# Kernel optimization log

Measured on AMD Instinct MI355X. Metric: run time of the kernel, lower is better.

The kernel has to match this reference:

```python
import jax, jax.numpy as jnp
import numpy as np

BSZ, L, P, H = 8, 8192, 128, 128


def setup_inputs() -> dict:
    key = jax.random.key(0)
    ks = jax.random.split(key, 7)
    x = jax.random.normal(ks[0], (BSZ, L, H), jnp.float32)
    A_diag = jax.random.uniform(ks[1], (P,), jnp.float32, 0.0, 2.0)
    G_diag = jax.random.uniform(ks[2], (P,), jnp.float32, 0.0, 1.0)
    dt = jax.random.normal(ks[3], (P,), jnp.float32)
    B = jax.random.uniform(ks[4], (P, H, 2), jnp.float32, -1.0, 1.0) / np.sqrt(H)
    C = jax.random.uniform(ks[5], (H, P, 2), jnp.float32, -1.0, 1.0) / np.sqrt(P)
    D = jax.random.normal(ks[6], (H,), jnp.float32)
    return {"x": x, "A_diag": A_diag, "G_diag": G_diag, "dt": dt, "B": B, "C": C, "D": D}


def _project_G(G, A, dt):
    # clamp G >= 0 and fold A into the valid stability interval [A_low, A_high]
    G = jnp.maximum(G, 0.0)
    dt2 = jnp.maximum(dt ** 2, 1e-06)
    s = jnp.sqrt(1.0 + dt * G)
    A_low = (2.0 + dt * G - 2.0 * s) / dt2
    A_high = (2.0 + dt * G + 2.0 * s) / dt2
    A_proj = A_low + jax.nn.relu(A - A_low) - jax.nn.relu(A - A_high)
    return A_proj, G


def _binop(q_i, q_j):
    # 2x2 block (per diagonal state p) recurrence composition: M_j @ M_i
    A_i, b_i = q_i
    A_j, b_j = q_j
    A_new = jnp.einsum('...ikp,...kjp->...ijp', A_j, A_i)
    b_new = jnp.einsum('...ikp,...kp->...ip', A_j, b_i) + b_j
    return A_new, b_new


def reference(x, A_diag, G_diag, dt, B, C, D):
    # _project_A_dt
    dt_s = jax.nn.sigmoid(dt)                       # (P,)
    A = jnp.maximum(A_diag, 0.0)
    # G_base = projected G given (A, dt)
    _, G_base = _project_G(G_diag, A, dt_s)
    # constant damping: G_seq is G_base broadcast over time, then re-projected per step
    G_seq = jnp.broadcast_to(G_base, (L, P))        # (L,P)
    A_seq, G_seq = _project_G(G_seq, A, dt_s)       # broadcasts over L
    A_fin = jnp.min(A_seq, axis=0)                  # (P,)
    # complex input projection Bu_k = B_complex @ u_k
    Bc = B[..., 0] + 1j * B[..., 1]                 # (P,H)
    Cc = C[..., 0] + 1j * C[..., 1]                 # (H,P)
    Bu = jnp.einsum('blh,ph->blp', x, Bc)           # (BSZ,L,P) complex64
    # IMEX transition coefficients
    S = 1.0 + dt_s * G_seq                          # (L,P)
    M11 = 1.0 / S
    M12 = -(dt_s / S) * A_fin
    M21 = dt_s / S
    M22 = 1.0 - (dt_s ** 2 / S) * A_fin
    M = jnp.stack([jnp.stack([M11, M12], axis=-2),
                   jnp.stack([M21, M22], axis=-2)], axis=-3)   # (L,2,2,P) real
    F = jnp.stack([(dt_s / S) * Bu, (dt_s ** 2 / S) * Bu], axis=-2)  # (BSZ,L,2,P) complex
    M_b = jnp.broadcast_to(M, (BSZ,) + M.shape)     # (BSZ,L,2,2,P)
    _, xs = jax.lax.associative_scan(_binop, (M_b, F), axis=1)
    ys = xs[..., 1, :]                              # (BSZ,L,P) complex: x-component
    out = jnp.einsum('blp,hp->blh', ys, Cc).real + D * x
    return out
```

## Files before the change

kernel.cpp:

```cpp
#include <hip/hip_runtime.h>
#include <math.h>

#define BSZ_ 8
#define LEN_ 8192
#define NC_  128
#define CT_  64

typedef __attribute__((ext_vector_type(8))) short bf16x8;
typedef __attribute__((ext_vector_type(4))) float f32x4;
typedef __attribute__((ext_vector_type(4))) unsigned short u16x4;
typedef __attribute__((ext_vector_type(8))) unsigned short u16x8;

#define OFF_PRM 0
#define OFF_W1T 2048
#define OFF_W2T (OFF_W1T + 16384)
#define OFF_MPW (OFF_W2T + 16384)
#define OFF_SUM (OFF_MPW + 16384)
#define OFF_V2  (OFF_SUM + BSZ_*NC_*256*2)

__device__ __forceinline__ unsigned short f2bf(float f) {
    unsigned u = __builtin_bit_cast(unsigned, f);
    u += 0x7fffu + ((u >> 16) & 1u);
    return (unsigned short)(u >> 16);
}

__device__ __forceinline__ unsigned short f2bf_fast(float f) {
    unsigned u = __builtin_bit_cast(unsigned, f);
    return (unsigned short)((u + 0x8000u) >> 16);
}

__device__ __forceinline__ float bf2f(unsigned short u) {
    return __builtin_bit_cast(float, (unsigned)u << 16);
}

__global__ __launch_bounds__(256) void k_setup(const float* __restrict__ A_diag,
                                               const float* __restrict__ G_diag,
                                               const float* __restrict__ dt,
                                               const float* __restrict__ B,
                                               const float* __restrict__ C,
                                               float* __restrict__ ws)
{
    int i = blockIdx.x * 256 + threadIdx.x;
    {
        int pc = i >> 7, h = i & 127;
        int p = pc >> 1, cc = pc & 1;
        float dts = 1.f / (1.f + expf(-dt[p]));
        float G = fmaxf(G_diag[p], 0.f);
        float c1 = dts / (1.f + dts * G);
        ((unsigned short*)(ws + OFF_W1T))[i] = f2bf(c1 * B[p * 256 + h * 2 + cc]);
    }
    {
        float v = C[i];
        ((unsigned short*)(ws + OFF_W2T))[i] = f2bf((i & 1) ? -v : v);
    }
    if (i < 8192) {
        int k = (i >> 7) + 1;
        int p = i & 127;
        float dtv = dt[p];
        float dts = 1.f / (1.f + expf(-dtv));
        float A   = fmaxf(A_diag[p], 0.f);
        float G   = fmaxf(G_diag[p], 0.f);
        float dt2 = fmaxf(dts * dts, 1e-6f);
        float s   = sqrtf(1.f + dts * G);
        float A_low  = (2.f + dts * G - 2.f * s) / dt2;
        float A_high = (2.f + dts * G + 2.f * s) / dt2;
        float Af = A_low + fmaxf(A - A_low, 0.f) - fmaxf(A - A_high, 0.f);
        float S   = 1.f + dts * G;
        float M11 = 1.f / S;
        float M12 = -(dts / S) * Af;
        float M21 = dts / S;
        float M22 = 1.f - (dts * dts / S) * Af;

        float r11 = 1.f, r12 = 0.f, r21 = 0.f, r22 = 1.f;
        float b11 = M11, b12 = M12, b21 = M21, b22 = M22;
        int kk = k;
#pragma unroll
        for (int it = 0; it < 7; ++it) {
            if (kk & 1) {
                float t11 = b11 * r11 + b12 * r21;
                float t12 = b11 * r12 + b12 * r22;
                float t21 = b21 * r11 + b22 * r21;
                float t22 = b21 * r12 + b22 * r22;
                r11 = t11; r12 = t12; r21 = t21; r22 = t22;
            }
            float s11 = b11 * b11 + b12 * b21;
            float s12 = b11 * b12 + b12 * b22;
            float s21 = b21 * b11 + b22 * b21;
            float s22 = b21 * b12 + b22 * b22;
            b11 = s11; b12 = s12; b21 = s21; b22 = s22;
            kk >>= 1;
        }
        float2* MPW = (float2*)(ws + OFF_MPW);
        MPW[(size_t)p * 64 + (k - 1)] = make_float2(r21, r22);

        float* prm = ws + OFF_PRM + p * 16;
        if (k == 1) {
            prm[0] = M11; prm[1] = M12; prm[2] = M21; prm[3] = M22; prm[4] = dts;
        }
        if (k == 64) {
            prm[5] = r11; prm[6] = r12; prm[7] = r21; prm[8] = r22;
            float u11 = r11, u12 = r12, u21 = r21, u22 = r22;
#pragma unroll
            for (int it = 0; it < 4; ++it) {
                float s11 = u11 * u11 + u12 * u21;
                float s12 = u11 * u12 + u12 * u22;
                float s21 = u21 * u11 + u22 * u21;
                float s22 = u21 * u12 + u22 * u22;
                u11 = s11; u12 = s12; u21 = s21; u22 = s22;
            }
            prm[9] = u11; prm[10] = u12; prm[11] = u21; prm[12] = u22;
        }
    }
}

__device__ __forceinline__ void stage_x(const float* __restrict__ X, size_t row0,
                                        int tid, unsigned short (*xs)[136])
{
    int r = tid >> 4, cl = (tid & 15) * 8;
#pragma unroll
    for (int i = 0; i < 4; ++i) {
        int rr = r + i * 16;
        const float* src = X + (row0 + rr) * 128 + cl;
        float4 v0 = *(const float4*)src;
        float4 v1 = *(const float4*)(src + 4);
        unsigned short* dst = &xs[rr][cl];
        dst[0] = f2bf_fast(v0.x); dst[1] = f2bf_fast(v0.y); dst[2] = f2bf_fast(v0.z); dst[3] = f2bf_fast(v0.w);
        dst[4] = f2bf_fast(v1.x); dst[5] = f2bf_fast(v1.y); dst[6] = f2bf_fast(v1.z); dst[7] = f2bf_fast(v1.w);
    }
}

__device__ __forceinline__ void gemm1_acc(const unsigned short (*xs)[136],
                                          const unsigned short* __restrict__ W1T,
                                          int wv, int lane, f32x4 acc[4][4])
{
    int l15 = lane & 15, quad = lane >> 4;
    int nbase = wv * 64;
#pragma unroll
    for (int kk = 0; kk < 4; ++kk) {
        int k0 = kk * 32 + quad * 8;
        bf16x8 af[4], bg[4];
#pragma unroll
        for (int mi = 0; mi < 4; ++mi) af[mi] = *(const bf16x8*)&xs[mi * 16 + l15][k0];
#pragma unroll
        for (int nj = 0; nj < 4; ++nj)
            bg[nj] = *(const bf16x8*)(W1T + (size_t)(nbase + nj * 16 + l15) * 128 + k0);
#pragma unroll
        for (int mi = 0; mi < 4; ++mi)
#pragma unroll
            for (int nj = 0; nj < 4; ++nj)
                acc[mi][nj] = __builtin_amdgcn_mfma_f32_16x16x32_bf16(af[mi], bg[nj], acc[mi][nj], 0, 0, 0);
    }
}

__global__ __launch_bounds__(256) void k_fuse1(const float* __restrict__ X,
                                               float* __restrict__ ws)
{
    __shared__ __align__(16) char smem[32 * 260 * 4];
    unsigned short (*xs)[136] = (unsigned short (*)[136])smem;
    float (*fl)[260] = (float (*)[260])smem;

    int tid = threadIdx.x;
    int b = blockIdx.x >> 7, c = blockIdx.x & 127;
    size_t row0 = (size_t)b * LEN_ + (size_t)c * CT_;

    stage_x(X, row0, tid, xs);
    __syncthreads();

    int wv = tid >> 6, lane = tid & 63;
    int l15 = lane & 15, quad = lane >> 4, nbase = wv * 64;
    f32x4 acc[4][4] = {};
    gemm1_acc(xs, (const unsigned short*)(ws + OFF_W1T), wv, lane, acc);
    __syncthreads();

    const float* prm = ws + OFF_PRM + (tid >> 1) * 16;
    float M11 = prm[0], M12 = prm[1], dts = prm[4];
    unsigned short* V2T = (unsigned short*)(ws + OFF_V2) +
                          (((size_t)b * NC_ + c) * 256 + tid) * 64;
    float h1 = 0.f, h2 = 0.f;

#pragma unroll
    for (int half = 0; half < 2; ++half) {
#pragma unroll
        for (int mi = 0; mi < 2; ++mi)
#pragma unroll
            for (int nj = 0; nj < 4; ++nj)
#pragma unroll
                for (int r = 0; r < 4; ++r)
                    fl[mi * 16 + quad * 4 + r][nbase + nj * 16 + l15] =
                        acc[half * 2 + mi][nj][r];
        __syncthreads();
#pragma unroll
        for (int g = 0; g < 8; ++g) {
            u16x4 pk;
#pragma unroll
            for (int i = 0; i < 4; ++i) {
                int t = g * 4 + i;
                float u = fl[t][tid];
                float n1 = fmaf(M11, h1, fmaf(M12, h2, u));
                float n2 = fmaf(dts, n1, h2);
                h1 = n1; h2 = n2;
                pk[i] = f2bf_fast(h2);
            }
            *(u16x4*)(V2T + half * 32 + g * 4) = pk;
        }
        __syncthreads();
    }
    *(float2*)(ws + OFF_SUM + (((size_t)b * NC_ + c) * 256 + tid) * 2) = make_float2(h1, h2);
}

__global__ __launch_bounds__(256) void k_scan2(float* __restrict__ ws)
{
    __shared__ float2 sums[32][8];
    int blk = blockIdx.x;
    int b = blk >> 3, chb = (blk & 7) * 32;
    int tid = threadIdx.x;
    int chl = tid >> 3, seg = tid & 7;
    int ch = chb + chl;
    const float* prm = ws + OFF_PRM + (ch >> 1) * 16;
    float T11 = prm[5], T12 = prm[6], T21 = prm[7], T22 = prm[8];
    float U11 = prm[9], U12 = prm[10], U21 = prm[11], U22 = prm[12];
    float* base = ws + OFF_SUM + (size_t)b * 65536 + ch * 2;

    float l1[16], l2[16];
    float s1 = 0.f, s2 = 0.f;
#pragma unroll
    for (int j = 0; j < 16; ++j) {
        float2 l = *(float2*)(base + (size_t)(seg * 16 + j) * 512);
        l1[j] = l.x; l2[j] = l.y;
        float n1 = fmaf(T11, s1, fmaf(T12, s2, l.x));
        float n2 = fmaf(T21, s1, fmaf(T22, s2, l.y));
        s1 = n1; s2 = n2;
    }
    sums[chl][seg] = make_float2(s1, s2);
    __syncthreads();

    if (seg == 0) {
        float e1 = 0.f, e2 = 0.f;
#pragma unroll
        for (int k = 0; k < 8; ++k) {
            float2 t = sums[chl][k];
            sums[chl][k] = make_float2(e1, e2);
            float n1 = fmaf(U11, e1, fmaf(U12, e2, t.x));
            float n2 = fmaf(U21, e1, fmaf(U22, e2, t.y));
            e1 = n1; e2 = n2;
        }
    }
    __syncthreads();

    float2 E = sums[chl][seg];
    float e1 = E.x, e2 = E.y;
#pragma unroll
    for (int j = 0; j < 16; ++j) {
        *(float2*)(base + (size_t)(seg * 16 + j) * 512) = make_float2(e1, e2);
        float n1 = fmaf(T11, e1, fmaf(T12, e2, l1[j]));
        float n2 = fmaf(T21, e1, fmaf(T22, e2, l2[j]));
        e1 = n1; e2 = n2;
    }
}

__global__ __launch_bounds__(256) void k_fuse2(const float* __restrict__ X,
                                               const float* __restrict__ Dv,
                                               float* __restrict__ ws,
                                               float* __restrict__ out)
{
    __shared__ __align__(16) unsigned short ysb[64][264];

    int tid = threadIdx.x;
    int b = blockIdx.x >> 7, c = blockIdx.x & 127;
    size_t row0 = (size_t)b * LEN_ + (size_t)c * CT_;

    {
        int q = tid & 127;
        int tseg = tid >> 7;
        float4 Cp = *(const float4*)(ws + OFF_SUM +
                                     (((size_t)b * NC_ + c) * 256 + 2 * q) * 2);
        const float2* MP = (const float2*)(ws + OFF_MPW) + (size_t)q * 64;
        const unsigned short* V2T = (const unsigned short*)(ws + OFF_V2) +
                                    (((size_t)b * NC_ + c) * 256 + 2 * q) * 64 + tseg * 32;
#pragma unroll
        for (int g = 0; g < 4; ++g) {
            u16x8 va = *(const u16x8*)(V2T + g * 8);
            u16x8 vb = *(const u16x8*)(V2T + 64 + g * 8);
#pragma unroll
            for (int i = 0; i < 4; ++i) {
                int tt = tseg * 32 + g * 8 + 2 * i;
                float4 mm = *(const float4*)(MP + tt);
                float y0 = fmaf(mm.x, Cp.x, fmaf(mm.y, Cp.y, bf2f(va[2 * i])));
                float y1 = fmaf(mm.x, Cp.z, fmaf(mm.y, Cp.w, bf2f(vb[2 * i])));
                *(ushort2*)&ysb[tt][2 * q] = make_ushort2(f2bf_fast(y0), f2bf_fast(y1));
                float y0b = fmaf(mm.z, Cp.x, fmaf(mm.w, Cp.y, bf2f(va[2 * i + 1])));
                float y1b = fmaf(mm.z, Cp.z, fmaf(mm.w, Cp.w, bf2f(vb[2 * i + 1])));
                *(ushort2*)&ysb[tt + 1][2 * q] = make_ushort2(f2bf_fast(y0b), f2bf_fast(y1b));
            }
        }
    }
    __syncthreads();

    int wv = tid >> 6, lane = tid & 63;
    int l15 = lane & 15, quad = lane >> 4;
    int mrow = (wv & 1) * 32, ncol = (wv >> 1) * 64;
    f32x4 a2[2][4] = {};
    const unsigned short* W2T = (const unsigned short*)(ws + OFF_W2T);
#pragma unroll
    for (int kk = 0; kk < 8; ++kk) {
        int k0 = kk * 32 + quad * 8;
        bf16x8 af[2], bg[4];
#pragma unroll
        for (int mi = 0; mi < 2; ++mi) af[mi] = *(const bf16x8*)&ysb[mrow + mi * 16 + l15][k0];
#pragma unroll
        for (int nj = 0; nj < 4; ++nj)
            bg[nj] = *(const bf16x8*)(W2T + (size_t)(ncol + nj * 16 + l15) * 256 + k0);
#pragma unroll
        for (int mi = 0; mi < 2; ++mi)
#pragma unroll
            for (int nj = 0; nj < 4; ++nj)
                a2[mi][nj] = __builtin_amdgcn_mfma_f32_16x16x32_bf16(af[mi], bg[nj], a2[mi][nj], 0, 0, 0);
    }

#pragma unroll
    for (int mi = 0; mi < 2; ++mi)
#pragma unroll
        for (int nj = 0; nj < 4; ++nj) {
            int col = ncol + nj * 16 + l15;
            float d = Dv[col];
#pragma unroll
            for (int r = 0; r < 4; ++r) {
                size_t gr = row0 + mrow + mi * 16 + quad * 4 + r;
                float xv = X[gr * 128 + col];
                out[gr * 128 + col] = fmaf(d, xv, a2[mi][nj][r]);
            }
        }
}

extern "C" void kernel_launch(void* const* d_in, const int* in_sizes, int n_in,
                              void* d_out, int out_size, void* d_ws, size_t ws_size,
                              hipStream_t stream) {
    const float* x      = (const float*)d_in[0];
    const float* A_diag = (const float*)d_in[1];
    const float* G_diag = (const float*)d_in[2];
    const float* dt     = (const float*)d_in[3];
    const float* B      = (const float*)d_in[4];
    const float* C      = (const float*)d_in[5];
    const float* Dv     = (const float*)d_in[6];
    float* out = (float*)d_out;
    float* ws  = (float*)d_ws;

    k_setup<<<128, 256, 0, stream>>>(A_diag, G_diag, dt, B, C, ws);
    k_fuse1<<<BSZ_ * NC_, 256, 0, stream>>>(x, ws);
    k_scan2<<<64, 256, 0, stream>>>(ws);
    k_fuse2<<<BSZ_ * NC_, 256, 0, stream>>>(x, Dv, ws, out);
}
```

Before: 153.3 us.

## Recompute input GEMM and local scan in second pass instead of storing intermediate states

The first pass no longer writes the per-timestep bf16 local states; it only computes the chunk-end summaries. The second pass restages x, redoes the first GEMM and local recurrence, and adds the carry-in correction on the fly before the output GEMM. This trades a large intermediate write and read through global memory for duplicated GEMM and scan compute in the second kernel. The MPW table layout is transposed to make per-timestep loads coalesced, and the scan2 thread mapping is changed for coalescing.

Measured after the change: 144.2 us. 1.06x faster.

```diff
diff --git a/kernel.cpp b/kernel.cpp
--- a/kernel.cpp
+++ b/kernel.cpp
@@ -8,15 +8,12 @@
 
 typedef __attribute__((ext_vector_type(8))) short bf16x8;
 typedef __attribute__((ext_vector_type(4))) float f32x4;
-typedef __attribute__((ext_vector_type(4))) unsigned short u16x4;
-typedef __attribute__((ext_vector_type(8))) unsigned short u16x8;
 
 #define OFF_PRM 0
 #define OFF_W1T 2048
 #define OFF_W2T (OFF_W1T + 16384)
 #define OFF_MPW (OFF_W2T + 16384)
-#define OFF_SUM (OFF_MPW + 16384)
-#define OFF_V2  (OFF_SUM + BSZ_*NC_*256*2)
+#define OFF_SUM (OFF_MPW + 16640)
 
 __device__ __forceinline__ unsigned short f2bf(float f) {
     unsigned u = __builtin_bit_cast(unsigned, f);
@@ -91,7 +88,7 @@
             kk >>= 1;
         }
         float2* MPW = (float2*)(ws + OFF_MPW);
-        MPW[(size_t)p * 64 + (k - 1)] = make_float2(r21, r22);
+        MPW[k * 128 + p] = make_float2(r21, r22);
 
         float* prm = ws + OFF_PRM + p * 16;
         if (k == 1) {
@@ -152,7 +149,7 @@
     }
 }
 
-__global__ __launch_bounds__(256) void k_fuse1(const float* __restrict__ X,
+__global__ __launch_bounds__(256) void k_part1(const float* __restrict__ X,
                                                float* __restrict__ ws)
 {
     __shared__ __align__(16) char smem[32 * 260 * 4];
@@ -174,8 +171,6 @@
 
     const float* prm = ws + OFF_PRM + (tid >> 1) * 16;
     float M11 = prm[0], M12 = prm[1], dts = prm[4];
-    unsigned short* V2T = (unsigned short*)(ws + OFF_V2) +
-                          (((size_t)b * NC_ + c) * 256 + tid) * 64;
     float h1 = 0.f, h2 = 0.f;
 
 #pragma unroll
@@ -189,19 +184,12 @@
                     fl[mi * 16 + quad * 4 + r][nbase + nj * 16 + l15] =
                         acc[half * 2 + mi][nj][r];
         __syncthreads();
-#pragma unroll
-        for (int g = 0; g < 8; ++g) {
-            u16x4 pk;
-#pragma unroll
-            for (int i = 0; i < 4; ++i) {
-                int t = g * 4 + i;
-                float u = fl[t][tid];
-                float n1 = fmaf(M11, h1, fmaf(M12, h2, u));
-                float n2 = fmaf(dts, n1, h2);
-                h1 = n1; h2 = n2;
-                pk[i] = f2bf_fast(h2);
-            }
-            *(u16x4*)(V2T + half * 32 + g * 4) = pk;
+#pragma unroll 8
+        for (int t = 0; t < 32; ++t) {
+            float u = fl[t][tid];
+            float n1 = fmaf(M11, h1, fmaf(M12, h2, u));
+            float n2 = fmaf(dts, n1, h2);
+            h1 = n1; h2 = n2;
         }
         __syncthreads();
     }
@@ -214,7 +202,7 @@
     int blk = blockIdx.x;
     int b = blk >> 3, chb = (blk & 7) * 32;
     int tid = threadIdx.x;
-    int chl = tid >> 3, seg = tid & 7;
+    int chl = tid & 31, seg = tid >> 5;
     int ch = chb + chl;
     const float* prm = ws + OFF_PRM + (ch >> 1) * 16;
     float T11 = prm[5], T12 = prm[6], T21 = prm[7], T22 = prm[8];
@@ -225,7 +213,7 @@
     float s1 = 0.f, s2 = 0.f;
 #pragma unroll
     for (int j = 0; j < 16; ++j) {
-        float2 l = *(float2*)(base + (size_t)(seg * 16 + j) * 512);
+        float2 l = *(const float2*)(base + (size_t)(seg * 16 + j) * 512);
         l1[j] = l.x; l2[j] = l.y;
         float n1 = fmaf(T11, s1, fmaf(T12, s2, l.x));
         float n2 = fmaf(T21, s1, fmaf(T22, s2, l.y));
@@ -234,12 +222,12 @@
     sums[chl][seg] = make_float2(s1, s2);
     __syncthreads();
 
-    if (seg == 0) {
+    if (tid < 32) {
         float e1 = 0.f, e2 = 0.f;
 #pragma unroll
         for (int k = 0; k < 8; ++k) {
-            float2 t = sums[chl][k];
-            sums[chl][k] = make_float2(e1, e2);
+            float2 t = sums[tid][k];
+            sums[tid][k] = make_float2(e1, e2);
             float n1 = fmaf(U11, e1, fmaf(U12, e2, t.x));
             float n2 = fmaf(U21, e1, fmaf(U22, e2, t.y));
             e1 = n1; e2 = n2;
@@ -258,46 +246,60 @@
     }
 }
 
-__global__ __launch_bounds__(256) void k_fuse2(const float* __restrict__ X,
-                                               const float* __restrict__ Dv,
-                                               float* __restrict__ ws,
-                                               float* __restrict__ out)
-{
+__global__ __launch_bounds__(256, 3) void k_part2(const float* __restrict__ X,
+                                                  const float* __restrict__ Dv,
+                                                  float* __restrict__ ws,
+                                                  float* __restrict__ out)
+{
+    __shared__ __align__(16) char smem1[64 * 136 * 2];
     __shared__ __align__(16) unsigned short ysb[64][264];
+
+    unsigned short (*xs)[136] = (unsigned short (*)[136])smem1;
+    float (*fl)[260] = (float (*)[260])smem1;
 
     int tid = threadIdx.x;
     int b = blockIdx.x >> 7, c = blockIdx.x & 127;
     size_t row0 = (size_t)b * LEN_ + (size_t)c * CT_;
 
-    {
-        int q = tid & 127;
-        int tseg = tid >> 7;
-        float4 Cp = *(const float4*)(ws + OFF_SUM +
-                                     (((size_t)b * NC_ + c) * 256 + 2 * q) * 2);
-        const float2* MP = (const float2*)(ws + OFF_MPW) + (size_t)q * 64;
-        const unsigned short* V2T = (const unsigned short*)(ws + OFF_V2) +
-                                    (((size_t)b * NC_ + c) * 256 + 2 * q) * 64 + tseg * 32;
-#pragma unroll
-        for (int g = 0; g < 4; ++g) {
-            u16x8 va = *(const u16x8*)(V2T + g * 8);
-            u16x8 vb = *(const u16x8*)(V2T + 64 + g * 8);
-#pragma unroll
-            for (int i = 0; i < 4; ++i) {
-                int tt = tseg * 32 + g * 8 + 2 * i;
-                float4 mm = *(const float4*)(MP + tt);
-                float y0 = fmaf(mm.x, Cp.x, fmaf(mm.y, Cp.y, bf2f(va[2 * i])));
-                float y1 = fmaf(mm.x, Cp.z, fmaf(mm.y, Cp.w, bf2f(vb[2 * i])));
-                *(ushort2*)&ysb[tt][2 * q] = make_ushort2(f2bf_fast(y0), f2bf_fast(y1));
-                float y0b = fmaf(mm.z, Cp.x, fmaf(mm.w, Cp.y, bf2f(va[2 * i + 1])));
-                float y1b = fmaf(mm.z, Cp.z, fmaf(mm.w, Cp.w, bf2f(vb[2 * i + 1])));
-                *(ushort2*)&ysb[tt + 1][2 * q] = make_ushort2(f2bf_fast(y0b), f2bf_fast(y1b));
-            }
-        }
-    }
+    stage_x(X, row0, tid, xs);
     __syncthreads();
 
     int wv = tid >> 6, lane = tid & 63;
-    int l15 = lane & 15, quad = lane >> 4;
+    int l15 = lane & 15, quad = lane >> 4, nbase = wv * 64;
+    f32x4 acc[4][4] = {};
+    gemm1_acc(xs, (const unsigned short*)(ws + OFF_W1T), wv, lane, acc);
+
+    float2 Cp = *(const float2*)(ws + OFF_SUM + (((size_t)b * NC_ + c) * 256 + tid) * 2);
+    const float* prm = ws + OFF_PRM + (tid >> 1) * 16;
+    float M11 = prm[0], M12 = prm[1], dts = prm[4];
+    const float2* MPW = (const float2*)(ws + OFF_MPW);
+    int p = tid >> 1;
+
+    __syncthreads();
+
+    float h1 = 0.f, h2 = 0.f;
+#pragma unroll
+    for (int q4 = 0; q4 < 4; ++q4) {
+#pragma unroll
+        for (int nj = 0; nj < 4; ++nj)
+#pragma unroll
+            for (int r = 0; r < 4; ++r)
+                fl[quad * 4 + r][nbase + nj * 16 + l15] = acc[q4][nj][r];
+        __syncthreads();
+#pragma unroll
+        for (int t = 0; t < 16; ++t) {
+            int tt = q4 * 16 + t;
+            float u = fl[t][tid];
+            float n1 = fmaf(M11, h1, fmaf(M12, h2, u));
+            float n2 = fmaf(dts, n1, h2);
+            h1 = n1; h2 = n2;
+            float2 m = MPW[(tt + 1) * 128 + p];
+            float y = fmaf(m.x, Cp.x, fmaf(m.y, Cp.y, n2));
+            ysb[tt][tid] = f2bf_fast(y);
+        }
+        __syncthreads();
+    }
+
     int mrow = (wv & 1) * 32, ncol = (wv >> 1) * 64;
     f32x4 a2[2][4] = {};
     const unsigned short* W2T = (const unsigned short*)(ws + OFF_W2T);
@@ -346,7 +348,7 @@
     float* ws  = (float*)d_ws;
 
     k_setup<<<128, 256, 0, stream>>>(A_diag, G_diag, dt, B, C, ws);
-    k_fuse1<<<BSZ_ * NC_, 256, 0, stream>>>(x, ws);
+    k_part1<<<BSZ_ * NC_, 256, 0, stream>>>(x, ws);
     k_scan2<<<64, 256, 0, stream>>>(ws);
-    k_fuse2<<<BSZ_ * NC_, 256, 0, stream>>>(x, Dv, ws, out);
-}
+    k_part2<<<BSZ_ * NC_, 256, 0, stream>>>(x, Dv, ws, out);
+}
```

## Interleave V2 and MPW workspace layouts for coalesced access across kernels

Applied to the files above, without the earlier changes.

Stores the per-chunk V2 intermediate in a time-quad-major layout (u16x4 per thread per 4-step group), so fuse1 writes and fuse2 reads become contiguous across threads instead of strided by 128 bytes. The MPW power table is reordered to [tq][p][4] so fuse2 loads it coalesced. scan2 remaps threads so consecutive lanes handle consecutive channels, which coalesces its strided sum loads and stores. Several kernels must agree on the new layouts, and any indexing mismatch would silently corrupt results.

After: 133.8 us. 1.15x faster.

```diff
diff --git a/kernel.cpp b/kernel.cpp
--- a/kernel.cpp
+++ b/kernel.cpp
@@ -16,7 +16,7 @@
 #define OFF_W2T (OFF_W1T + 16384)
 #define OFF_MPW (OFF_W2T + 16384)
 #define OFF_SUM (OFF_MPW + 16384)
-#define OFF_V2  (OFF_SUM + BSZ_*NC_*256*2)
+#define OFF_V2  (OFF_SUM + 524288)
 
 __device__ __forceinline__ unsigned short f2bf(float f) {
     unsigned u = __builtin_bit_cast(unsigned, f);
@@ -90,8 +90,11 @@
             b11 = s11; b12 = s12; b21 = s21; b22 = s22;
             kk >>= 1;
         }
-        float2* MPW = (float2*)(ws + OFF_MPW);
-        MPW[(size_t)p * 64 + (k - 1)] = make_float2(r21, r22);
+        {
+            int tq = (k - 1) >> 2, j = (k - 1) & 3;
+            ((float2*)(ws + OFF_MPW))[((size_t)tq * 128 + p) * 4 + j] =
+                make_float2(r21, r22);
+        }
 
         float* prm = ws + OFF_PRM + p * 16;
         if (k == 1) {
@@ -160,7 +163,8 @@
     float (*fl)[260] = (float (*)[260])smem;
 
     int tid = threadIdx.x;
-    int b = blockIdx.x >> 7, c = blockIdx.x & 127;
+    int bc = blockIdx.x;
+    int b = bc >> 7, c = bc & 127;
     size_t row0 = (size_t)b * LEN_ + (size_t)c * CT_;
 
     stage_x(X, row0, tid, xs);
@@ -174,8 +178,7 @@
 
     const float* prm = ws + OFF_PRM + (tid >> 1) * 16;
     float M11 = prm[0], M12 = prm[1], dts = prm[4];
-    unsigned short* V2T = (unsigned short*)(ws + OFF_V2) +
-                          (((size_t)b * NC_ + c) * 256 + tid) * 64;
+    u16x4* V2q = (u16x4*)(ws + OFF_V2) + (size_t)bc * 4096;
     float h1 = 0.f, h2 = 0.f;
 
 #pragma unroll
@@ -194,18 +197,17 @@
             u16x4 pk;
 #pragma unroll
             for (int i = 0; i < 4; ++i) {
-                int t = g * 4 + i;
-                float u = fl[t][tid];
+                float u = fl[g * 4 + i][tid];
                 float n1 = fmaf(M11, h1, fmaf(M12, h2, u));
                 float n2 = fmaf(dts, n1, h2);
                 h1 = n1; h2 = n2;
                 pk[i] = f2bf_fast(h2);
             }
-            *(u16x4*)(V2T + half * 32 + g * 4) = pk;
+            V2q[(half * 8 + g) * 256 + tid] = pk;
         }
         __syncthreads();
     }
-    *(float2*)(ws + OFF_SUM + (((size_t)b * NC_ + c) * 256 + tid) * 2) = make_float2(h1, h2);
+    *(float2*)(ws + OFF_SUM + (((size_t)bc) * 256 + tid) * 2) = make_float2(h1, h2);
 }
 
 __global__ __launch_bounds__(256) void k_scan2(float* __restrict__ ws)
@@ -214,7 +216,7 @@
     int blk = blockIdx.x;
     int b = blk >> 3, chb = (blk & 7) * 32;
     int tid = threadIdx.x;
-    int chl = tid >> 3, seg = tid & 7;
+    int chl = tid & 31, seg = tid >> 5;
     int ch = chb + chl;
     const float* prm = ws + OFF_PRM + (ch >> 1) * 16;
     float T11 = prm[5], T12 = prm[6], T21 = prm[7], T22 = prm[8];
@@ -225,7 +227,7 @@
     float s1 = 0.f, s2 = 0.f;
 #pragma unroll
     for (int j = 0; j < 16; ++j) {
-        float2 l = *(float2*)(base + (size_t)(seg * 16 + j) * 512);
+        float2 l = *(const float2*)(base + (size_t)(seg * 16 + j) * 512);
         l1[j] = l.x; l2[j] = l.y;
         float n1 = fmaf(T11, s1, fmaf(T12, s2, l.x));
         float n2 = fmaf(T21, s1, fmaf(T22, s2, l.y));
@@ -234,12 +236,12 @@
     sums[chl][seg] = make_float2(s1, s2);
     __syncthreads();
 
-    if (seg == 0) {
+    if (tid < 32) {
         float e1 = 0.f, e2 = 0.f;
 #pragma unroll
         for (int k = 0; k < 8; ++k) {
-            float2 t = sums[chl][k];
-            sums[chl][k] = make_float2(e1, e2);
+            float2 t = sums[tid][k];
+            sums[tid][k] = make_float2(e1, e2);
             float n1 = fmaf(U11, e1, fmaf(U12, e2, t.x));
             float n2 = fmaf(U21, e1, fmaf(U22, e2, t.y));
             e1 = n1; e2 = n2;
@@ -266,32 +268,38 @@
     __shared__ __align__(16) unsigned short ysb[64][264];
 
     int tid = threadIdx.x;
-    int b = blockIdx.x >> 7, c = blockIdx.x & 127;
+    int bc = blockIdx.x;
+    int b = bc >> 7, c = bc & 127;
     size_t row0 = (size_t)b * LEN_ + (size_t)c * CT_;
 
     {
         int q = tid & 127;
         int tseg = tid >> 7;
-        float4 Cp = *(const float4*)(ws + OFF_SUM +
-                                     (((size_t)b * NC_ + c) * 256 + 2 * q) * 2);
-        const float2* MP = (const float2*)(ws + OFF_MPW) + (size_t)q * 64;
-        const unsigned short* V2T = (const unsigned short*)(ws + OFF_V2) +
-                                    (((size_t)b * NC_ + c) * 256 + 2 * q) * 64 + tseg * 32;
-#pragma unroll
-        for (int g = 0; g < 4; ++g) {
-            u16x8 va = *(const u16x8*)(V2T + g * 8);
-            u16x8 vb = *(const u16x8*)(V2T + 64 + g * 8);
-#pragma unroll
-            for (int i = 0; i < 4; ++i) {
-                int tt = tseg * 32 + g * 8 + 2 * i;
-                float4 mm = *(const float4*)(MP + tt);
-                float y0 = fmaf(mm.x, Cp.x, fmaf(mm.y, Cp.y, bf2f(va[2 * i])));
-                float y1 = fmaf(mm.x, Cp.z, fmaf(mm.y, Cp.w, bf2f(vb[2 * i])));
-                *(ushort2*)&ysb[tt][2 * q] = make_ushort2(f2bf_fast(y0), f2bf_fast(y1));
-                float y0b = fmaf(mm.z, Cp.x, fmaf(mm.w, Cp.y, bf2f(va[2 * i + 1])));
-                float y1b = fmaf(mm.z, Cp.z, fmaf(mm.w, Cp.w, bf2f(vb[2 * i + 1])));
-                *(ushort2*)&ysb[tt + 1][2 * q] = make_ushort2(f2bf_fast(y0b), f2bf_fast(y1b));
-            }
+        float4 Cp = *(const float4*)(ws + OFF_SUM + ((size_t)bc * 256 + 2 * q) * 2);
+        const unsigned short* V2b = (const unsigned short*)(ws + OFF_V2) +
+                                    (size_t)bc * 16384;
+        const float2* MPW = (const float2*)(ws + OFF_MPW);
+#pragma unroll
+        for (int g = 0; g < 8; ++g) {
+            int tq = tseg * 8 + g;
+            u16x8 v = *(const u16x8*)(V2b + (size_t)tq * 1024 + 8 * q);
+            const float2* MP = MPW + ((size_t)tq * 128 + q) * 4;
+            float4 mA = *(const float4*)MP;
+            float4 mB = *(const float4*)(MP + 2);
+            int t0 = tq * 4;
+            float y0, y1;
+            y0 = fmaf(mA.x, Cp.x, fmaf(mA.y, Cp.y, bf2f(v[0])));
+            y1 = fmaf(mA.x, Cp.z, fmaf(mA.y, Cp.w, bf2f(v[4])));
+            *(ushort2*)&ysb[t0 + 0][2 * q] = make_ushort2(f2bf_fast(y0), f2bf_fast(y1));
+            y0 = fmaf(mA.z, Cp.x, fmaf(mA.w, Cp.y, bf2f(v[1])));
+            y1 = fmaf(mA.z, Cp.z, fmaf(mA.w, Cp.w, bf2f(v[5])));
+            *(ushort2*)&ysb[t0 + 1][2 * q] = make_ushort2(f2bf_fast(y0), f2bf_fast(y1));
+            y0 = fmaf(mB.x, Cp.x, fmaf(mB.y, Cp.y, bf2f(v[2])));
+            y1 = fmaf(mB.x, Cp.z, fmaf(mB.y, Cp.w, bf2f(v[6])));
+            *(ushort2*)&ysb[t0 + 2][2 * q] = make_ushort2(f2bf_fast(y0), f2bf_fast(y1));
+            y0 = fmaf(mB.z, Cp.x, fmaf(mB.w, Cp.y, bf2f(v[3])));
+            y1 = fmaf(mB.z, Cp.z, fmaf(mB.w, Cp.w, bf2f(v[7])));
+            *(ushort2*)&ysb[t0 + 3][2 * q] = make_ushort2(f2bf_fast(y0), f2bf_fast(y1));
         }
     }
     __syncthreads();
```
